# Performance work log

Measured on AMD Instinct MI355X. Metric: run time of the kernel, lower is better.

## Reference

```python
import math
import jax, jax.numpy as jnp
import numpy as np

D_MODEL = 1024
N_HEADS = 16
D_HEAD = D_MODEL // N_HEADS
ROPE_BASE = 10000.0
MAX_SEQ_LEN = 2048


def build_cos_sin_cache(d_head, max_seq_len, base=ROPE_BASE):
    half = d_head // 2
    i = jnp.arange(half, dtype=jnp.float32)
    theta = 1.0 / (base ** (2.0 * i / d_head))  # (half,)
    t = jnp.arange(max_seq_len, dtype=jnp.float32)
    angles = jnp.outer(t, theta)  # (T, half)
    return jnp.cos(angles), jnp.sin(angles)


def rotate_half(x):
    d = x.shape[-1]
    x1, x2 = x[..., : d // 2], x[..., d // 2 :]
    return jnp.concatenate([-x2, x1], axis=-1)


def apply_rope(x, cos_t, sin_t):
    # x: (..., T, d_head); cos_t/sin_t: (T, d_head//2)
    cos_full = jnp.concatenate([cos_t, cos_t], axis=-1)
    sin_full = jnp.concatenate([sin_t, sin_t], axis=-1)
    return x * cos_full + rotate_half(x) * sin_full


def setup_inputs() -> dict:
    key = jax.random.key(0)
    ks = jax.random.split(key, 5)
    B, T = 2, 2048
    s = 1.0 / math.sqrt(D_MODEL)
    return {
        "x": jax.random.normal(ks[0], (B, T, D_MODEL), dtype=jnp.float32),
        "Wq": jax.random.normal(ks[1], (D_MODEL, D_MODEL), dtype=jnp.float32) * s,
        "Wk": jax.random.normal(ks[2], (D_MODEL, D_MODEL), dtype=jnp.float32) * s,
        "Wv": jax.random.normal(ks[3], (D_MODEL, D_MODEL), dtype=jnp.float32) * s,
        "Wo": jax.random.normal(ks[4], (D_MODEL, D_MODEL), dtype=jnp.float32) * s,
    }


def reference(x, Wq, Wk, Wv, Wo):
    B, T, _ = x.shape
    # Linear with torch weight convention: y = x @ W.T
    q = jnp.einsum("btd,ed->bte", x, Wq)
    k = jnp.einsum("btd,ed->bte", x, Wk)
    v = jnp.einsum("btd,ed->bte", x, Wv)
    # (B, H, T, d_head)
    q = q.reshape(B, T, N_HEADS, D_HEAD).transpose(0, 2, 1, 3)
    k = k.reshape(B, T, N_HEADS, D_HEAD).transpose(0, 2, 1, 3)
    v = v.reshape(B, T, N_HEADS, D_HEAD).transpose(0, 2, 1, 3)
    cos_c, sin_c = build_cos_sin_cache(D_HEAD, MAX_SEQ_LEN)
    cos_t, sin_t = cos_c[:T], sin_c[:T]
    q = apply_rope(q, cos_t, sin_t)
    k = apply_rope(k, cos_t, sin_t)
    scale = math.sqrt(D_HEAD)
    scores = jnp.einsum("bhqd,bhkd->bhqk", q, k) / scale
    causal = jnp.triu(jnp.full((T, T), -jnp.inf, dtype=x.dtype), k=1)
    scores = scores + causal
    weights = jax.nn.softmax(scores, axis=-1)
    out = jnp.einsum("bhqk,bhkd->bhqd", weights, v)
    out = out.transpose(0, 2, 1, 3).reshape(B, T, D_MODEL)
    return jnp.einsum("btd,ed->bte", out, Wo)
```

## Files before the change

### kernel.cpp

```cpp
#include <hip/hip_runtime.h>
#include <stdint.h>
#include <math.h>

typedef __attribute__((ext_vector_type(8))) short short8;
typedef __attribute__((ext_vector_type(4))) float f32x4;
typedef __attribute__((ext_vector_type(16))) float f32x16;

#define T_SEQ 2048
#define MROWS 4096
#define LOG2E 1.44269504088896f

#define OFF_XBF   ((size_t)0)
#define OFF_WQ    ((size_t)8388608)
#define OFF_WK    ((size_t)10485760)
#define OFF_WV    ((size_t)12582912)
#define OFF_WO    ((size_t)14680064)
#define OFF_Q     ((size_t)16777216)
#define OFF_K     ((size_t)25165824)
#define OFF_VT    ((size_t)33554432)
#define OFF_ATT   ((size_t)41943040)
#define OFF_COS   ((size_t)50331648)
#define OFF_SIN   ((size_t)50593792)
#define OFF_OPART ((size_t)0)
#define OFF_ML    ((size_t)12582912)

__device__ __forceinline__ unsigned short f2bf(float f) {
  unsigned u = __float_as_uint(f);
  u += 0x7fffu + ((u >> 16) & 1u);
  return (unsigned short)(u >> 16);
}

__device__ __forceinline__ float bf2f(unsigned short u) {
  return __uint_as_float((unsigned)u << 16);
}

__device__ __forceinline__ void gld_lds16(const void* g, void* l) {
  __builtin_amdgcn_global_load_lds(
      (__attribute__((address_space(1))) void*)(g),
      (__attribute__((address_space(3))) void*)(l), 16, 0, 0);
}

__device__ __forceinline__ unsigned cvt_pk_bf16(float lo, float hi) {
  unsigned r;
  asm("v_cvt_pk_bf16_f32 %0, %1, %2" : "=v"(r) : "v"(lo), "v"(hi));
  return r;
}

__global__ void prep_kernel(const float* x, const float* wq, const float* wk,
                            const float* wv, const float* wo, char* ws) {
  const size_t NX4 = (size_t)MROWS * 1024 / 4;
  const size_t NW4 = (size_t)1024 * 1024 / 4;
  const size_t NT = (size_t)T_SEQ * 32;
  unsigned short* xb = (unsigned short*)(ws + OFF_XBF);
  unsigned short* wqb = (unsigned short*)(ws + OFF_WQ);
  unsigned short* wkb = (unsigned short*)(ws + OFF_WK);
  unsigned short* wvb = (unsigned short*)(ws + OFF_WV);
  unsigned short* wob = (unsigned short*)(ws + OFF_WO);
  float* cosb = (float*)(ws + OFF_COS);
  float* sinb = (float*)(ws + OFF_SIN);
  size_t nvec = NX4 + 4 * NW4;
  size_t total = nvec + NT;
  for (size_t i = (size_t)blockIdx.x * blockDim.x + threadIdx.x; i < total;
       i += (size_t)gridDim.x * blockDim.x) {
    if (i < nvec) {
      const float* src;
      unsigned short* dst;
      size_t e;
      if (i < NX4) {
        src = x; dst = xb; e = i * 4;
      } else {
        size_t j = i - NX4;
        int wsel = (int)(j / NW4);
        e = (j - (size_t)wsel * NW4) * 4;
        src = wsel == 0 ? wq : wsel == 1 ? wk : wsel == 2 ? wv : wo;
        dst = wsel == 0 ? wqb : wsel == 1 ? wkb : wsel == 2 ? wvb : wob;
      }
      float4 v = *(const float4*)(src + e);
      unsigned long long p =
          (unsigned long long)f2bf(v.x) |
          ((unsigned long long)f2bf(v.y) << 16) |
          ((unsigned long long)f2bf(v.z) << 32) |
          ((unsigned long long)f2bf(v.w) << 48);
      *(unsigned long long*)(dst + e) = p;
    } else {
      size_t j = i - nvec;
      int t = (int)(j >> 5), ii = (int)(j & 31);
      double th = exp(-(double)ii * (9.210340371976184 / 32.0));
      float ang = (float)t * (float)th;
      cosb[j] = cosf(ang);
      sinb[j] = sinf(ang);
    }
  }
}

__global__ __launch_bounds__(256, 3) void gemm_qkv(
    const unsigned short* Abf, const unsigned short* Wall, unsigned short* qkout,
    unsigned short* vtout, const float* cosT, const float* sinT) {
  const int K = 1024;
  int bid0 = blockIdx.x;
  int bid = (bid0 & 7) * 96 + (bid0 >> 3);
  int bm = bid / 24, bn = bid % 24;
  int sel = bn >> 3, bnc = bn & 7;
  int tid = threadIdx.x;
  int l = tid & 63, w = tid >> 6;
  int wm = w >> 1, wn = w & 1;
  int g = l >> 4;

  __shared__ __align__(16) char ldsbuf[32768];

  auto stage = [&](int kt, int buf) {
    int base = buf * 16384;
#pragma unroll
    for (int i = 0; i < 2; ++i) {
      int p = (w * 2 + i) * 1024;
      int row = (p >> 6) + (l >> 2);
      int u = l & 3;
      const char* ga = (const char*)Abf +
          ((size_t)(bm * 128 + row) * K + (size_t)kt * 32) * 2 + u * 16;
      gld_lds16(ga, ldsbuf + base + p);
      const char* gb = (const char*)Wall +
          ((size_t)(bn * 128 + row) * K + (size_t)kt * 32) * 2 + u * 16;
      gld_lds16(gb, ldsbuf + base + 8192 + p);
    }
  };

  f32x4 acc[4][4] = {};
  stage(0, 0);
  const int nk = K / 32;
  for (int kt = 0; kt < nk; ++kt) {
    int buf = kt & 1;
    if (kt + 1 < nk) {
      stage(kt + 1, buf ^ 1);
      asm volatile("s_waitcnt vmcnt(4)" ::: "memory");
    } else {
      asm volatile("s_waitcnt vmcnt(0)" ::: "memory");
    }
    __builtin_amdgcn_s_barrier();
    __builtin_amdgcn_sched_barrier(0);
    const char* Ab = ldsbuf + buf * 16384;
    const char* Bb = Ab + 8192;
    short8 af[4], bfr[4];
#pragma unroll
    for (int m = 0; m < 4; ++m)
      af[m] = *(const short8*)(Ab + (wm * 64 + m * 16 + (l & 15)) * 64 + g * 16);
#pragma unroll
    for (int n = 0; n < 4; ++n)
      bfr[n] = *(const short8*)(Bb + (wn * 64 + n * 16 + (l & 15)) * 64 + g * 16);
#pragma unroll
    for (int m = 0; m < 4; ++m)
#pragma unroll
      for (int n = 0; n < 4; ++n)
        acc[m][n] = __builtin_amdgcn_mfma_f32_16x16x32_bf16(af[m], bfr[n],
                                                            acc[m][n], 0, 0, 0);
    __builtin_amdgcn_s_barrier();
  }

  int row0 = bm * 128 + wm * 64;
  int col0 = bnc * 128 + wn * 64;
  if (sel < 2) {
    float qscale = sel == 0 ? 0.125f * LOG2E : 1.0f;
    unsigned short* C = qkout + (size_t)sel * MROWS * 1024;
#pragma unroll
    for (int m = 0; m < 4; ++m)
#pragma unroll
      for (int n = 0; n < 2; ++n)
#pragma unroll
        for (int r = 0; r < 4; ++r) {
          int row = row0 + m * 16 + g * 4 + r;
          int t = row & (T_SEQ - 1);
          int d = n * 16 + (l & 15);
          float c = cosT[t * 32 + d], s = sinT[t * 32 + d];
          float v0 = acc[m][n][r], v1 = acc[m][n + 2][r];
          C[(size_t)row * 1024 + col0 + d] = f2bf((v0 * c - v1 * s) * qscale);
          C[(size_t)row * 1024 + col0 + d + 32] = f2bf((v1 * c + v0 * s) * qscale);
        }
  } else {
    unsigned short* C = vtout;
#pragma unroll
    for (int m = 0; m < 4; ++m) {
      int rowb = row0 + m * 16 + g * 4;
      int bb = rowb >> 11, t0 = rowb & (T_SEQ - 1);
#pragma unroll
      for (int n = 0; n < 4; ++n) {
        int e = col0 + n * 16 + (l & 15);
        unsigned long long pv =
            (unsigned long long)f2bf(acc[m][n][0]) |
            ((unsigned long long)f2bf(acc[m][n][1]) << 16) |
            ((unsigned long long)f2bf(acc[m][n][2]) << 32) |
            ((unsigned long long)f2bf(acc[m][n][3]) << 48);
        *(unsigned long long*)(C + ((size_t)bb * 1024 + e) * T_SEQ + t0) = pv;
      }
    }
  }
}

__global__ __launch_bounds__(256, 3) void gemm_wo(const unsigned short* Abf,
                                                  const unsigned short* Wbf,
                                                  float* out) {
  const int K = 1024, N = 1024;
  int bid0 = blockIdx.x;
  int bid = (bid0 & 7) * 64 + (bid0 >> 3);
  int bm = bid >> 4, bn = bid & 15;
  int tid = threadIdx.x;
  int l = tid & 63, w = tid >> 6;
  int wm = w >> 1, wn = w & 1;
  int g = l >> 4;

  __shared__ __align__(16) char ldsbuf[24576];

  auto stage = [&](int kt, int buf) {
    char* base = ldsbuf + buf * 12288;
#pragma unroll
    for (int i = 0; i < 2; ++i) {
      int pos = tid + i * 256;
      int row = pos >> 2, u = pos & 3;
      const char* ga = (const char*)Abf +
          ((size_t)(bm * 128 + row) * K + (size_t)kt * 32) * 2 + u * 16;
      gld_lds16(ga, base + row * 64 + u * 16);
    }
    {
      int row = tid >> 2, u = tid & 3;
      const char* gb = (const char*)Wbf +
          ((size_t)(bn * 64 + row) * K + (size_t)kt * 32) * 2 + u * 16;
      gld_lds16(gb, base + 8192 + row * 64 + u * 16);
    }
  };

  f32x4 acc[4][2] = {};
  stage(0, 0);
  const int nk = K / 32;
  for (int kt = 0; kt < nk; ++kt) {
    int buf = kt & 1;
    if (kt + 1 < nk) {
      stage(kt + 1, buf ^ 1);
      asm volatile("s_waitcnt vmcnt(3)" ::: "memory");
    } else {
      asm volatile("s_waitcnt vmcnt(0)" ::: "memory");
    }
    __builtin_amdgcn_s_barrier();
    __builtin_amdgcn_sched_barrier(0);
    const char* Ab = ldsbuf + buf * 12288;
    const char* Bb = Ab + 8192;
    short8 af[4], bfr[2];
#pragma unroll
    for (int m = 0; m < 4; ++m)
      af[m] = *(const short8*)(Ab + (wm * 64 + m * 16 + (l & 15)) * 64 + g * 16);
#pragma unroll
    for (int n = 0; n < 2; ++n)
      bfr[n] = *(const short8*)(Bb + (wn * 32 + n * 16 + (l & 15)) * 64 + g * 16);
#pragma unroll
    for (int m = 0; m < 4; ++m)
#pragma unroll
      for (int n = 0; n < 2; ++n)
        acc[m][n] = __builtin_amdgcn_mfma_f32_16x16x32_bf16(af[m], bfr[n],
                                                            acc[m][n], 0, 0, 0);
    __builtin_amdgcn_s_barrier();
  }

  int row0 = bm * 128 + wm * 64;
  int col0 = bn * 64 + wn * 32;
#pragma unroll
  for (int m = 0; m < 4; ++m)
#pragma unroll
    for (int n = 0; n < 2; ++n)
#pragma unroll
      for (int r = 0; r < 4; ++r)
        out[(size_t)(row0 + m * 16 + g * 4 + r) * N + col0 + n * 16 + (l & 15)] =
            acc[m][n][r];
}

__global__ __launch_bounds__(128, 2) void attn_kernel(
    const unsigned short* Qbf, const unsigned short* Kbf,
    const unsigned short* VT, unsigned short* att,
    unsigned short* Opart, float* lpart) {
  static const unsigned char remap[30] = {
      5, 16, 17, 14, 15, 28, 29, 4, 12, 13, 23, 24, 25, 26, 27,
      10, 11, 19, 20, 21, 22, 3, 8, 9, 18, 6, 7, 2, 1, 0};
  int bid = blockIdx.x;
  int bh = bid & 31;
  int cid = remap[bid >> 5];
  int b = bh >> 4, h = bh & 15;
  int qt, s, ns;
  if (cid < 6) {
    qt = cid; s = 0; ns = 1;
  } else if (cid < 18) {
    int e = cid - 6; qt = 6 + (e >> 1); s = e & 1; ns = 2;
  } else {
    int e = cid - 18; qt = 12 + e / 3; s = e - 3 * (e / 3); ns = 3;
  }
  int ntt_full = 2 * qt + 2;
  int kt0 = (s * ntt_full) / ns;
  int ntt = ((s + 1) * ntt_full) / ns - kt0;
  int pbi = bh * 24 + (ns == 2 ? (cid - 6) : (cid - 18 + 12));

  int tid = threadIdx.x;
  int l = tid & 63, w = tid >> 6;
  int q32 = l & 31, hi = l >> 5;
  int q0 = qt * 128;
  int q0w = q0 + w * 64;
  int ntw = (((q0w + 63) >> 6) + 1) - kt0;
  if (ntw > ntt) ntw = ntt;
  if (ntw < 0) ntw = 0;

  __shared__ __align__(16) char lds[2][16384];

  short8 qfA[4], qfB[4];
  {
    const char* qb = (const char*)Qbf +
        ((size_t)(b * T_SEQ + q0w + q32)) * 2048 + h * 128 + hi * 16;
#pragma unroll
    for (int ks = 0; ks < 4; ++ks) {
      qfA[ks] = *(const short8*)(qb + ks * 32);
      qfB[ks] = *(const short8*)(qb + 32 * 2048 + ks * 32);
    }
  }
  asm volatile("s_waitcnt vmcnt(0)" ::: "memory");

  auto stage = [&](int gt, int buf) {
    char* Kd = &lds[buf][0];
    char* Vd = &lds[buf][8192];
    int colb = (tid & 7) * 16;
#pragma unroll
    for (int r = 0; r < 4; ++r) {
      int d = (tid >> 3) + r * 16;
      int sc = colb ^ ((d & 7) << 4);
      const char* gk = (const char*)Kbf +
          ((size_t)(b * T_SEQ + gt * 64 + d)) * 2048 + h * 128 + sc;
      gld_lds16(gk, Kd + d * 128 + colb);
      const char* gv = (const char*)VT +
          ((size_t)(b * 1024 + h * 64 + d)) * 4096 + gt * 128 + sc;
      gld_lds16(gv, Vd + d * 128 + colb);
    }
  };

  f32x16 oA0 = {}, oA1 = {}, oB0 = {}, oB1 = {};
  float lA = 0.f, lB = 0.f;
  stage(kt0, 0);
  for (int kt = 0; kt < ntt; ++kt) {
    int buf = kt & 1;
    if (kt + 1 < ntt) {
      stage(kt0 + kt + 1, buf ^ 1);
      asm volatile("s_waitcnt vmcnt(8)" ::: "memory");
    } else {
      asm volatile("s_waitcnt vmcnt(0)" ::: "memory");
    }
    __builtin_amdgcn_s_barrier();
    __builtin_amdgcn_sched_barrier(0);
    if (kt < ntw) {
      int gt = kt0 + kt;
      const char* Kl = &lds[buf][0];
      const char* Vl = &lds[buf][8192];

      f32x16 sA0 = {}, sA1 = {}, sB0 = {}, sB1 = {};
      __builtin_amdgcn_s_setprio(1);
#pragma unroll
      for (int ks = 0; ks < 4; ++ks) {
        int sc = (ks * 32 + hi * 16) ^ ((q32 & 7) << 4);
        short8 k0 = *(const short8*)(Kl + q32 * 128 + sc);
        short8 k1 = *(const short8*)(Kl + (q32 + 32) * 128 + sc);
        sA0 = __builtin_amdgcn_mfma_f32_32x32x16_bf16(k0, qfA[ks], sA0, 0, 0, 0);
        sA1 = __builtin_amdgcn_mfma_f32_32x32x16_bf16(k1, qfA[ks], sA1, 0, 0, 0);
        sB0 = __builtin_amdgcn_mfma_f32_32x32x16_bf16(k0, qfB[ks], sB0, 0, 0, 0);
        sB1 = __builtin_amdgcn_mfma_f32_32x32x16_bf16(k1, qfB[ks], sB1, 0, 0, 0);
      }
      __builtin_amdgcn_s_setprio(0);

      if (gt * 64 + 63 > q0w) {
        int qA = q0w + q32, qB = qA + 32;
#pragma unroll
        for (int r = 0; r < 16; ++r) {
          int kkb = gt * 64 + (r & 3) + 8 * (r >> 2) + 4 * hi;
          if (kkb > qA) sA0[r] = -1e30f;
          if (kkb + 32 > qA) sA1[r] = -1e30f;
          if (kkb > qB) sB0[r] = -1e30f;
          if (kkb + 32 > qB) sB1[r] = -1e30f;
        }
      }

      float lsA = 0.f, lsB = 0.f;
#pragma unroll
      for (int r = 0; r < 16; ++r) {
        sA0[r] = __builtin_amdgcn_exp2f(sA0[r]);
        sA1[r] = __builtin_amdgcn_exp2f(sA1[r]);
        sB0[r] = __builtin_amdgcn_exp2f(sB0[r]);
        sB1[r] = __builtin_amdgcn_exp2f(sB1[r]);
        lsA += sA0[r] + sA1[r];
        lsB += sB0[r] + sB1[r];
      }
      lsA += __shfl_xor(lsA, 32);
      lsB += __shfl_xor(lsB, 32);
      lA += lsA;
      lB += lsB;

      short8 pbA[4], pbB[4];
#pragma unroll
      for (int ks = 0; ks < 4; ++ks) {
        union { unsigned u[4]; short8 s8; } ua, ub;
#pragma unroll
        for (int j = 0; j < 4; ++j) {
          int bse = (ks & 1) * 8 + 2 * j;
          float a0 = (ks & 2) ? sA1[bse] : sA0[bse];
          float a1 = (ks & 2) ? sA1[bse + 1] : sA0[bse + 1];
          ua.u[j] = cvt_pk_bf16(a0, a1);
          float b0 = (ks & 2) ? sB1[bse] : sB0[bse];
          float b1 = (ks & 2) ? sB1[bse + 1] : sB0[bse + 1];
          ub.u[j] = cvt_pk_bf16(b0, b1);
        }
        pbA[ks] = ua.s8;
        pbB[ks] = ub.s8;
      }

      __builtin_amdgcn_s_setprio(1);
#pragma unroll
      for (int ks = 0; ks < 4; ++ks) {
        int sp = (q32 & 7) << 4;
        int cA = (ks * 32 + 8 * hi) ^ sp;
        int cB = (ks * 32 + 16 + 8 * hi) ^ sp;
#pragma unroll
        for (int cc = 0; cc < 2; ++cc) {
          int dv = cc * 32 + q32;
          union { unsigned long long u[2]; short8 s8; } vv;
          vv.u[0] = *(const unsigned long long*)(Vl + dv * 128 + cA);
          vv.u[1] = *(const unsigned long long*)(Vl + dv * 128 + cB);
          if (cc == 0) {
            oA0 = __builtin_amdgcn_mfma_f32_32x32x16_bf16(vv.s8, pbA[ks], oA0, 0, 0, 0);
            oB0 = __builtin_amdgcn_mfma_f32_32x32x16_bf16(vv.s8, pbB[ks], oB0, 0, 0, 0);
          } else {
            oA1 = __builtin_amdgcn_mfma_f32_32x32x16_bf16(vv.s8, pbA[ks], oA1, 0, 0, 0);
            oB1 = __builtin_amdgcn_mfma_f32_32x32x16_bf16(vv.s8, pbB[ks], oB1, 0, 0, 0);
          }
        }
      }
      __builtin_amdgcn_s_setprio(0);
    }
    __builtin_amdgcn_s_barrier();
  }

  float scA = (ns == 1) ? (1.0f / lA) : 1.0f;
  float scB = (ns == 1) ? (1.0f / lB) : 1.0f;
  if (ns > 1 && hi == 0) {
    lpart[(size_t)pbi * 128 + w * 64 + q32] = lA;
    lpart[(size_t)pbi * 128 + w * 64 + 32 + q32] = lB;
  }
  __syncthreads();
  float* Ol = (float*)lds;
#pragma unroll
  for (int grp = 0; grp < 2; ++grp)
#pragma unroll
    for (int cc = 0; cc < 2; ++cc)
#pragma unroll
      for (int r = 0; r < 16; ++r) {
        int d = cc * 32 + (r & 3) + 8 * (r >> 2) + 4 * hi;
        float v;
        if (grp == 0) v = (cc ? oA1[r] : oA0[r]) * scA;
        else          v = (cc ? oB1[r] : oB0[r]) * scB;
        Ol[(w * 2 + grp) * 2048 + q32 * 64 + (d ^ (q32 & 31))] = v;
      }
  __syncthreads();
#pragma unroll
  for (int i = 0; i < 8; ++i) {
    int idx2 = tid + i * 128;
    int row = idx2 >> 3;
    int seg = idx2 & 7;
    int q = row & 31, rg = row >> 5;
    unsigned short tmp[8];
#pragma unroll
    for (int j = 0; j < 8; ++j) {
      int d = seg * 8 + j;
      tmp[j] = f2bf(Ol[rg * 2048 + q * 64 + (d ^ (q & 31))]);
    }
    if (ns == 1) {
      *(unsigned long long*)(att + ((size_t)(b * T_SEQ + q0 + row)) * 1024 +
                             h * 64 + seg * 8) = *(unsigned long long*)&tmp[0];
      *(unsigned long long*)(att + ((size_t)(b * T_SEQ + q0 + row)) * 1024 +
                             h * 64 + seg * 8 + 4) = *(unsigned long long*)&tmp[4];
    } else {
      *(unsigned long long*)(Opart + ((size_t)pbi * 128 + row) * 64 + seg * 8) =
          *(unsigned long long*)&tmp[0];
      *(unsigned long long*)(Opart + ((size_t)pbi * 128 + row) * 64 + seg * 8 + 4) =
          *(unsigned long long*)&tmp[4];
    }
  }
}

__global__ __launch_bounds__(256) void combine_kernel(
    const unsigned short* Opart, const float* lpart, unsigned short* att) {
  int blk = blockIdx.x;
  int bh = blk & 31, j = blk >> 5;
  int qt = 6 + j;
  int b = bh >> 4, h = bh & 15;
  int q0 = qt * 128;
  int ns = qt < 12 ? 2 : 3;
  int base = qt < 12 ? (qt - 6) * 2 : 12 + (qt - 12) * 3;
  int pbi0 = bh * 24 + base;
#pragma unroll
  for (int i = 0; i < 4; ++i) {
    int u = threadIdx.x + i * 256;
    int q = u >> 3, seg = u & 7;
    float lsum = 0.f;
#pragma unroll
    for (int p = 0; p < 3; ++p)
      if (p < ns) lsum += lpart[(size_t)(pbi0 + p) * 128 + q];
    float inv = 1.0f / lsum;
    float accv[8] = {};
#pragma unroll
    for (int p = 0; p < 3; ++p) {
      if (p < ns) {
        short8 ov = *(const short8*)(Opart +
            ((size_t)(pbi0 + p) * 128 + q) * 64 + seg * 8);
#pragma unroll
        for (int k = 0; k < 8; ++k)
          accv[k] += bf2f((unsigned short)ov[k]);
      }
    }
    union { unsigned short us[8]; short8 s8; } r;
#pragma unroll
    for (int k = 0; k < 8; ++k) r.us[k] = f2bf(accv[k] * inv);
    *(short8*)(att + ((size_t)(b * T_SEQ + q0 + q)) * 1024 + h * 64 + seg * 8) =
        r.s8;
  }
}

extern "C" void kernel_launch(void* const* d_in, const int* in_sizes, int n_in,
                              void* d_out, int out_size, void* d_ws,
                              size_t ws_size, hipStream_t stream) {
  const float* x = (const float*)d_in[0];
  const float* Wq = (const float*)d_in[1];
  const float* Wk = (const float*)d_in[2];
  const float* Wv = (const float*)d_in[3];
  const float* Wo = (const float*)d_in[4];
  char* ws = (char*)d_ws;

  unsigned short* xb = (unsigned short*)(ws + OFF_XBF);
  unsigned short* wall = (unsigned short*)(ws + OFF_WQ);
  unsigned short* wob = (unsigned short*)(ws + OFF_WO);
  unsigned short* qbf = (unsigned short*)(ws + OFF_Q);
  unsigned short* vtb = (unsigned short*)(ws + OFF_VT);
  unsigned short* att = (unsigned short*)(ws + OFF_ATT);
  unsigned short* kbf = (unsigned short*)(ws + OFF_K);
  unsigned short* opart = (unsigned short*)(ws + OFF_OPART);
  float* lp = (float*)(ws + OFF_ML);
  const float* cosT = (const float*)(ws + OFF_COS);
  const float* sinT = (const float*)(ws + OFF_SIN);

  prep_kernel<<<2048, 256, 0, stream>>>(x, Wq, Wk, Wv, Wo, ws);
  gemm_qkv<<<768, 256, 0, stream>>>(xb, wall, qbf, vtb, cosT, sinT);
  attn_kernel<<<960, 128, 0, stream>>>(qbf, kbf, vtb, att, opart, lp);
  combine_kernel<<<320, 256, 0, stream>>>(opart, lp, att);
  gemm_wo<<<512, 256, 0, stream>>>(att, wob, (float*)d_out);
}
```

Before: 105.1 us.

## Split attention KV range across two warp-pairs per block with in-LDS reduction

Attention blocks grow from 128 to 256 threads. Two independent 2-wave groups each process half of a work item's key tiles and merge their partial O and l sums through LDS. Cross-block splitting is cut to at most 2 parts (qt>=8), with a fixed query-tile ordering table, fewer blocks and a simpler combine kernel. The aim is to reduce inter-block partial writes and combine traffic while keeping enough parallelism, at the cost of extra LDS use, more syncs and a larger block footprint.

```diff
diff --git a/kernel.cpp b/kernel.cpp
--- a/kernel.cpp
+++ b/kernel.cpp
@@ -269,40 +269,44 @@
             acc[m][n][r];
 }
 
-__global__ __launch_bounds__(128, 2) void attn_kernel(
+__global__ __launch_bounds__(256, 2) void attn_kernel(
     const unsigned short* Qbf, const unsigned short* Kbf,
     const unsigned short* VT, unsigned short* att,
     unsigned short* Opart, float* lpart) {
-  static const unsigned char remap[30] = {
-      5, 16, 17, 14, 15, 28, 29, 4, 12, 13, 23, 24, 25, 26, 27,
-      10, 11, 19, 20, 21, 22, 3, 8, 9, 18, 6, 7, 2, 1, 0};
+  static const unsigned char qtab[24] = {15, 15, 14, 14, 7,  13, 13, 12,
+                                         12, 6,  11, 11, 10, 10, 5,  9,
+                                         9,  8,  8,  4,  3,  2,  1,  0};
+  static const unsigned char stab[24] = {0,   1,   0,   1,   255, 0,   1,   0,
+                                         1,   255, 0,   1,   0,   1,   255, 0,
+                                         1,   0,   1,   255, 255, 255, 255, 255};
   int bid = blockIdx.x;
   int bh = bid & 31;
-  int cid = remap[bid >> 5];
+  int cid = bid >> 5;
+  int qt = qtab[cid];
+  int sv = stab[cid];
+  int ns = (sv == 255) ? 1 : 2;
+  int s = (sv == 255) ? 0 : sv;
   int b = bh >> 4, h = bh & 15;
-  int qt, s, ns;
-  if (cid < 6) {
-    qt = cid; s = 0; ns = 1;
-  } else if (cid < 18) {
-    int e = cid - 6; qt = 6 + (e >> 1); s = e & 1; ns = 2;
-  } else {
-    int e = cid - 18; qt = 12 + e / 3; s = e - 3 * (e / 3); ns = 3;
-  }
-  int ntt_full = 2 * qt + 2;
-  int kt0 = (s * ntt_full) / ns;
-  int ntt = ((s + 1) * ntt_full) / ns - kt0;
-  int pbi = bh * 24 + (ns == 2 ? (cid - 6) : (cid - 18 + 12));
+  int ntt = 2 * qt + 2;
+  int ntb = (ns == 2) ? (ntt >> 1) : ntt;
+  int kt0 = s * ntb;
+  int hp = (ntb + 1) >> 1;
 
   int tid = threadIdx.x;
-  int l = tid & 63, w = tid >> 6;
+  int pr = tid >> 7;
+  int t127 = tid & 127;
+  int l = tid & 63, wv = (tid >> 6) & 1;
   int q32 = l & 31, hi = l >> 5;
   int q0 = qt * 128;
-  int q0w = q0 + w * 64;
-  int ntw = (((q0w + 63) >> 6) + 1) - kt0;
-  if (ntw > ntt) ntw = ntt;
+  int q0w = q0 + wv * 64;
+  int myCnt = pr ? (ntb - hp) : hp;
+  int myKt0 = kt0 + (pr ? hp : 0);
+  int ntw = ((q0w + 63) >> 6) + 1 - myKt0;
+  if (ntw > myCnt) ntw = myCnt;
   if (ntw < 0) ntw = 0;
-
-  __shared__ __align__(16) char lds[2][16384];
+  int pbi = (ns == 2) ? (bh * 16 + (qt - 8) * 2 + s) : 0;
+
+  __shared__ __align__(16) char lds[2][2][16384];
 
   short8 qfA[4], qfB[4];
   {
@@ -317,12 +321,12 @@
   asm volatile("s_waitcnt vmcnt(0)" ::: "memory");
 
   auto stage = [&](int gt, int buf) {
-    char* Kd = &lds[buf][0];
-    char* Vd = &lds[buf][8192];
-    int colb = (tid & 7) * 16;
+    char* Kd = &lds[pr][buf][0];
+    char* Vd = &lds[pr][buf][8192];
+    int colb = (t127 & 7) * 16;
 #pragma unroll
     for (int r = 0; r < 4; ++r) {
-      int d = (tid >> 3) + r * 16;
+      int d = (t127 >> 3) + r * 16;
       int sc = colb ^ ((d & 7) << 4);
       const char* gk = (const char*)Kbf +
           ((size_t)(b * T_SEQ + gt * 64 + d)) * 2048 + h * 128 + sc;
@@ -335,21 +339,21 @@
 
   f32x16 oA0 = {}, oA1 = {}, oB0 = {}, oB1 = {};
   float lA = 0.f, lB = 0.f;
-  stage(kt0, 0);
-  for (int kt = 0; kt < ntt; ++kt) {
-    int buf = kt & 1;
-    if (kt + 1 < ntt) {
-      stage(kt0 + kt + 1, buf ^ 1);
+  stage(myKt0, 0);
+  for (int it = 0; it < hp; ++it) {
+    int buf = it & 1;
+    if (it + 1 < myCnt) {
+      stage(myKt0 + it + 1, buf ^ 1);
       asm volatile("s_waitcnt vmcnt(8)" ::: "memory");
     } else {
       asm volatile("s_waitcnt vmcnt(0)" ::: "memory");
     }
     __builtin_amdgcn_s_barrier();
     __builtin_amdgcn_sched_barrier(0);
-    if (kt < ntw) {
-      int gt = kt0 + kt;
-      const char* Kl = &lds[buf][0];
-      const char* Vl = &lds[buf][8192];
+    if (it < ntw) {
+      int gt = myKt0 + it;
+      const char* Kl = &lds[pr][buf][0];
+      const char* Vl = &lds[pr][buf][8192];
 
       f32x16 sA0 = {}, sA1 = {}, sB0 = {}, sB1 = {};
       __builtin_amdgcn_s_setprio(1);
@@ -387,8 +391,6 @@
         lsA += sA0[r] + sA1[r];
         lsB += sB0[r] + sB1[r];
       }
-      lsA += __shfl_xor(lsA, 32);
-      lsB += __shfl_xor(lsB, 32);
       lA += lsA;
       lB += lsB;
 
@@ -436,30 +438,72 @@
     __builtin_amdgcn_s_barrier();
   }
 
-  float scA = (ns == 1) ? (1.0f / lA) : 1.0f;
-  float scB = (ns == 1) ? (1.0f / lB) : 1.0f;
-  if (ns > 1 && hi == 0) {
-    lpart[(size_t)pbi * 128 + w * 64 + q32] = lA;
-    lpart[(size_t)pbi * 128 + w * 64 + 32 + q32] = lB;
-  }
+  lA += __shfl_xor(lA, 32);
+  lB += __shfl_xor(lB, 32);
+
+  float* M = (float*)(&lds[1][0][0]);
+  float* Ll = (float*)(&lds[0][0][0]);
   __syncthreads();
-  float* Ol = (float*)lds;
-#pragma unroll
-  for (int grp = 0; grp < 2; ++grp)
-#pragma unroll
-    for (int cc = 0; cc < 2; ++cc)
-#pragma unroll
-      for (int r = 0; r < 16; ++r) {
-        int d = cc * 32 + (r & 3) + 8 * (r >> 2) + 4 * hi;
-        float v;
-        if (grp == 0) v = (cc ? oA1[r] : oA0[r]) * scA;
-        else          v = (cc ? oB1[r] : oB0[r]) * scB;
-        Ol[(w * 2 + grp) * 2048 + q32 * 64 + (d ^ (q32 & 31))] = v;
-      }
+  if (pr == 1) {
+#pragma unroll
+    for (int grp = 0; grp < 2; ++grp)
+#pragma unroll
+      for (int cc = 0; cc < 2; ++cc)
+#pragma unroll
+        for (int r = 0; r < 16; ++r) {
+          int d = cc * 32 + (r & 3) + 8 * (r >> 2) + 4 * hi;
+          float v = grp == 0 ? (cc ? oA1[r] : oA0[r]) : (cc ? oB1[r] : oB0[r]);
+          M[(wv * 2 + grp) * 2048 + q32 * 64 + (d ^ (q32 & 31))] = v;
+        }
+    if (hi == 0) {
+      Ll[wv * 128 + q32] = lA;
+      Ll[wv * 128 + 64 + q32] = lB;
+    }
+  }
   __syncthreads();
-#pragma unroll
-  for (int i = 0; i < 8; ++i) {
-    int idx2 = tid + i * 128;
+  if (pr == 0) {
+#pragma unroll
+    for (int grp = 0; grp < 2; ++grp)
+#pragma unroll
+      for (int cc = 0; cc < 2; ++cc)
+#pragma unroll
+        for (int r = 0; r < 16; ++r) {
+          int d = cc * 32 + (r & 3) + 8 * (r >> 2) + 4 * hi;
+          float v = M[(wv * 2 + grp) * 2048 + q32 * 64 + (d ^ (q32 & 31))];
+          if (grp == 0) { if (cc) oA1[r] += v; else oA0[r] += v; }
+          else          { if (cc) oB1[r] += v; else oB0[r] += v; }
+        }
+    lA += Ll[wv * 128 + q32];
+    lB += Ll[wv * 128 + 64 + q32];
+  }
+  __syncthreads();
+
+  float* Ol = (float*)(&lds[0][0][0]);
+  if (pr == 0) {
+    float scA = (ns == 1) ? (1.0f / lA) : 1.0f;
+    float scB = (ns == 1) ? (1.0f / lB) : 1.0f;
+    if (ns > 1 && hi == 0) {
+      lpart[(size_t)pbi * 128 + wv * 64 + q32] = lA;
+      lpart[(size_t)pbi * 128 + wv * 64 + 32 + q32] = lB;
+    }
+#pragma unroll
+    for (int grp = 0; grp < 2; ++grp)
+#pragma unroll
+      for (int cc = 0; cc < 2; ++cc)
+#pragma unroll
+        for (int r = 0; r < 16; ++r) {
+          int d = cc * 32 + (r & 3) + 8 * (r >> 2) + 4 * hi;
+          float v;
+          if (grp == 0) v = (cc ? oA1[r] : oA0[r]) * scA;
+          else          v = (cc ? oB1[r] : oB0[r]) * scB;
+          Ol[(wv * 2 + grp) * 2048 + q32 * 64 + (d ^ (q32 & 31))] = v;
+        }
+  }
+  __syncthreads();
+
+#pragma unroll
+  for (int i = 0; i < 4; ++i) {
+    int idx2 = tid + i * 256;
     int row = idx2 >> 3;
     int seg = idx2 & 7;
     int q = row & 31, rg = row >> 5;
@@ -487,35 +531,25 @@
     const unsigned short* Opart, const float* lpart, unsigned short* att) {
   int blk = blockIdx.x;
   int bh = blk & 31, j = blk >> 5;
-  int qt = 6 + j;
+  int qt = 8 + j;
   int b = bh >> 4, h = bh & 15;
   int q0 = qt * 128;
-  int ns = qt < 12 ? 2 : 3;
-  int base = qt < 12 ? (qt - 6) * 2 : 12 + (qt - 12) * 3;
-  int pbi0 = bh * 24 + base;
+  int pbi0 = bh * 16 + j * 2;
 #pragma unroll
   for (int i = 0; i < 4; ++i) {
     int u = threadIdx.x + i * 256;
     int q = u >> 3, seg = u & 7;
-    float lsum = 0.f;
-#pragma unroll
-    for (int p = 0; p < 3; ++p)
-      if (p < ns) lsum += lpart[(size_t)(pbi0 + p) * 128 + q];
+    float lsum = lpart[(size_t)pbi0 * 128 + q] +
+                 lpart[(size_t)(pbi0 + 1) * 128 + q];
     float inv = 1.0f / lsum;
-    float accv[8] = {};
-#pragma unroll
-    for (int p = 0; p < 3; ++p) {
-      if (p < ns) {
-        short8 ov = *(const short8*)(Opart +
-            ((size_t)(pbi0 + p) * 128 + q) * 64 + seg * 8);
-#pragma unroll
-        for (int k = 0; k < 8; ++k)
-          accv[k] += bf2f((unsigned short)ov[k]);
-      }
-    }
+    short8 o0 = *(const short8*)(Opart + ((size_t)pbi0 * 128 + q) * 64 + seg * 8);
+    short8 o1 =
+        *(const short8*)(Opart + ((size_t)(pbi0 + 1) * 128 + q) * 64 + seg * 8);
     union { unsigned short us[8]; short8 s8; } r;
 #pragma unroll
-    for (int k = 0; k < 8; ++k) r.us[k] = f2bf(accv[k] * inv);
+    for (int k = 0; k < 8; ++k)
+      r.us[k] = f2bf((bf2f((unsigned short)o0[k]) +
+                      bf2f((unsigned short)o1[k])) * inv);
     *(short8*)(att + ((size_t)(b * T_SEQ + q0 + q)) * 1024 + h * 64 + seg * 8) =
         r.s8;
   }
@@ -545,7 +579,7 @@
 
   prep_kernel<<<2048, 256, 0, stream>>>(x, Wq, Wk, Wv, Wo, ws);
   gemm_qkv<<<768, 256, 0, stream>>>(xb, wall, qbf, vtb, cosT, sinT);
-  attn_kernel<<<960, 128, 0, stream>>>(qbf, kbf, vtb, att, opart, lp);
-  combine_kernel<<<320, 256, 0, stream>>>(opart, lp, att);
+  attn_kernel<<<768, 256, 0, stream>>>(qbf, kbf, vtb, att, opart, lp);
+  combine_kernel<<<256, 256, 0, stream>>>(opart, lp, att);
   gemm_wo<<<512, 256, 0, stream>>>(att, wob, (float*)d_out);
 }
```

Result: no change. 104.9 us (-0.2%).
